# Performance work log

Measured on AMD Instinct MI355X. Metric: run time of the kernel, lower is better.

The kernel has to match this reference:

```python
import jax, jax.numpy as jnp
import numpy as np

EPS = 1e-12  # torch F.normalize eps

def _l2norm(t):
    # normalize over last axis (N), clamp norm like torch.nn.functional.normalize
    n = jnp.linalg.norm(t, axis=-1, keepdims=True)
    return t / jnp.maximum(n, EPS)

def setup_inputs() -> dict:
    key = jax.random.key(0)
    ks = jax.random.split(key, 4)
    B, N, D, H = 8, 4096, 768, 16
    x = jax.random.normal(ks[0], (B, N, D), dtype=jnp.float32)
    w_qkv = jax.random.normal(ks[1], (D, 3 * D), dtype=jnp.float32) * (D ** -0.5)
    temperature = jnp.ones((H, 1, 1), dtype=jnp.float32)
    w_proj = jax.random.normal(ks[2], (D, D), dtype=jnp.float32) * (D ** -0.5)
    b_proj = jnp.zeros((D,), dtype=jnp.float32)
    return {"x": x, "w_qkv": w_qkv, "temperature": temperature,
            "w_proj": w_proj, "b_proj": b_proj}

def reference(x, w_qkv, temperature, w_proj, b_proj):
    B, N, D = x.shape
    H = temperature.shape[0]
    C = D // H
    # qkv linear (no bias), split last dim as (3, H, C), move to (3, B, H, C, N)
    qkv = (x @ w_qkv).reshape(B, N, 3, H, C).transpose(2, 0, 3, 4, 1)
    q, k, v = qkv[0], qkv[1], qkv[2]            # each [B, H, C, N]
    q = _l2norm(q)
    k = _l2norm(k)
    # cross-covariance attention: small CxC matrix per head
    attn = jnp.einsum('bhcn,bhdn->bhcd', q, k) * temperature  # [B,H,C,C]
    attn = jax.nn.softmax(attn, axis=-1)
    out = jnp.einsum('bhcd,bhdn->bhcn', attn, v)  # [B,H,C,N]
    out = out.transpose(0, 3, 1, 2).reshape(B, N, D)  # B N (H C)
    return out @ w_proj + b_proj
```

## Files before the change

### kernel.cpp

```cpp
#include <hip/hip_runtime.h>
#include <stdint.h>

typedef __attribute__((ext_vector_type(4))) float          f32x4;
typedef __attribute__((ext_vector_type(8))) short          bf16x8;
typedef __attribute__((ext_vector_type(8))) unsigned short u16x8;
typedef __attribute__((ext_vector_type(4))) unsigned short u16x4;

static __device__ __forceinline__ unsigned short f2bf(float f){
  uint32_t u = __builtin_bit_cast(uint32_t, f);
  u += 0x7FFFu + ((u >> 16) & 1u);
  return (unsigned short)(u >> 16);
}
static __device__ __forceinline__ float bf2f(unsigned short h){
  uint32_t u = ((uint32_t)h) << 16;
  return __builtin_bit_cast(float, u);
}

#define GLL(SRC, DST) __builtin_amdgcn_global_load_lds(                         \
    (const __attribute__((address_space(1))) unsigned int*)(SRC),               \
    (__attribute__((address_space(3))) unsigned int*)(DST), 16, 0, 0)

__global__ void k_cvt(const float* __restrict__ in, unsigned short* __restrict__ out, long n){
  long i = ((long)blockIdx.x * blockDim.x + threadIdx.x) * 8;
  if (i >= n) return;
  const f32x4* p = (const f32x4*)(in + i);
  f32x4 a = p[0], b = p[1];
  u16x8 o;
  #pragma unroll
  for (int j = 0; j < 4; j++){ o[j] = f2bf(a[j]); o[4+j] = f2bf(b[j]); }
  *(u16x8*)(out + i) = o;
}

__global__ void k_tconv(const float* __restrict__ in, unsigned short* __restrict__ out, int R, int C){
  __shared__ float tl[64][65];
  const int c0 = blockIdx.x * 64, r0 = blockIdx.y * 64;
  const int t = threadIdx.x;
  {
    const int lr = t >> 2, lc = (t & 3) * 16;
    const f32x4* s = (const f32x4*)(in + (long)(r0 + lr) * C + c0 + lc);
    #pragma unroll
    for (int q = 0; q < 4; q++){
      f32x4 v = s[q];
      #pragma unroll
      for (int j = 0; j < 4; j++) tl[lr][lc + q*4 + j] = v[j];
    }
  }
  __syncthreads();
  {
    const int oc = t >> 2, orr = (t & 3) * 16;
    u16x8 o0, o1;
    #pragma unroll
    for (int i = 0; i < 8; i++){ o0[i] = f2bf(tl[orr + i][oc]); o1[i] = f2bf(tl[orr + 8 + i][oc]); }
    u16x8* dst = (u16x8*)(out + (long)(c0 + oc) * R + r0 + orr);
    dst[0] = o0; dst[1] = o1;
  }
}

__global__ void k_cvtwv(const float* __restrict__ w, unsigned short* __restrict__ out){
  const long idx = ((long)blockIdx.x * blockDim.x + threadIdx.x) * 8;
  const int e = (int)(idx / 768), hd = (int)(idx - (long)e * 768);
  const float* s = w + (long)e * 2304 + 1536 + hd;
  f32x4 a = *(const f32x4*)s, b = *(const f32x4*)(s + 4);
  u16x8 o;
  #pragma unroll
  for (int j = 0; j < 4; j++){ o[j] = f2bf(a[j]); o[4+j] = f2bf(b[j]); }
  *(u16x8*)(out + idx) = o;
}

static __device__ __forceinline__ bf16x8 ldfrag(const char* slot, int row, int ko){
  const int k2 = (ko ^ (row >> 1)) & 3;
  return *(const bf16x8*)(slot + row*64 + k2*16);
}

static __device__ __forceinline__ void stg256(const unsigned short* __restrict__ G, int row0, int ke,
                                              char* lds_slot, int t){
  #pragma unroll
  for (int l = 0; l < 2; l++){
    const int r  = l*128 + (t >> 2);
    const int k2 = (t & 3) ^ ((r >> 1) & 3);
    GLL((const char*)(G + (long)(row0 + r) * 768 + ke + k2 * 8),
        lds_slot + l*8192 + (t & 0x1C0) * 16);
  }
}

#define PHASE(BUF, KK, MH, STAGE_STMT, WAIT_STMT) do {                         \
    bf16x8 af[4];                                                              \
    if (MH == 0) {                                                             \
      _Pragma("unroll")                                                        \
      for (int ni = 0; ni < 4; ni++)                                           \
        bq[ni] = ldfrag(sB[BUF][KK], wn*64 + ni*16 + arow, ko);                \
    }                                                                          \
    _Pragma("unroll")                                                          \
    for (int mi = 0; mi < 4; mi++)                                             \
      af[mi] = ldfrag(sA[BUF][KK], wm*128 + MH*64 + mi*16 + arow, ko);         \
    __builtin_amdgcn_s_barrier();                                              \
    __builtin_amdgcn_s_setprio(1);                                             \
    _Pragma("unroll")                                                          \
    for (int mi = 0; mi < 4; mi++)                                             \
      _Pragma("unroll")                                                        \
      for (int ni = 0; ni < 4; ni++)                                           \
        acc[MH*4+mi][ni] = __builtin_amdgcn_mfma_f32_16x16x32_bf16(            \
            af[mi], bq[ni], acc[MH*4+mi][ni], 0, 0, 0);                        \
    __builtin_amdgcn_s_setprio(0);                                             \
    STAGE_STMT;                                                                \
    WAIT_STMT;                                                                 \
    __builtin_amdgcn_s_barrier();                                              \
  } while(0)

__global__ __launch_bounds__(512, 2)
void k_gemm256(const unsigned short* __restrict__ A, const unsigned short* __restrict__ BT,
               unsigned short* __restrict__ QT, unsigned short* __restrict__ KT,
               float* __restrict__ nrmp)
{
  __shared__ __attribute__((aligned(16))) char lds[131072];
  const int o  = blockIdx.x;
  const int wg = (o & 7) * 96 + (o >> 3);
  const int jt = wg % 6, mt = wg / 6;
  const int m0 = mt * 256, j0 = jt * 256;
  const int t = threadIdx.x, lane = t & 63, w = t >> 6;
  const int wm = w >> 2, wn = w & 3;
  const int arow = lane & 15, ko = lane >> 4;

  char* const sA[2][2] = {{lds,           lds + 16384},
                          {lds + 65536,   lds + 65536 + 16384}};
  char* const sB[2][2] = {{lds + 32768,   lds + 49152},
                          {lds + 65536 + 32768, lds + 65536 + 49152}};

  f32x4 acc[8][4] = {};

  stg256(BT, j0, 0,   sB[0][0], t);
  stg256(A,  m0, 0,   sA[0][0], t);
  stg256(BT, j0, 32,  sB[0][1], t);
  stg256(A,  m0, 32,  sA[0][1], t);
  stg256(BT, j0, 64,  sB[1][0], t);
  stg256(A,  m0, 64,  sA[1][0], t);
  stg256(BT, j0, 96,  sB[1][1], t);
  asm volatile("s_waitcnt vmcnt(6)" ::: "memory");
  __builtin_amdgcn_s_barrier();

  #pragma unroll 1
  for (int it = 0; it < 6; ++it){
    const int t1 = 2*it + 1, t2 = 2*it + 2, t3 = 2*it + 3;
    bf16x8 bq[4];
    PHASE(0,0,0, { stg256(A, m0, t1*64+32, sA[1][1], t); }, ;);
    PHASE(0,0,1, { if (t2 < 12) stg256(BT, j0, t2*64,    sB[0][0], t); }, ;);
    PHASE(0,1,0, { if (t2 < 12) stg256(A,  m0, t2*64,    sA[0][0], t); }, ;);
    PHASE(0,1,1, { if (t2 < 12) stg256(BT, j0, t2*64+32, sB[0][1], t); },
                 { if (it == 5) asm volatile("s_waitcnt vmcnt(0)" ::: "memory");
                   else         asm volatile("s_waitcnt vmcnt(6)" ::: "memory"); });
    PHASE(1,0,0, { if (t2 < 12) stg256(A,  m0, t2*64+32, sA[0][1], t); }, ;);
    PHASE(1,0,1, { if (t3 < 12) stg256(BT, j0, t3*64,    sB[1][0], t); }, ;);
    PHASE(1,1,0, { if (t3 < 12) stg256(A,  m0, t3*64,    sA[1][0], t); }, ;);
    PHASE(1,1,1, { if (t3 < 12) stg256(BT, j0, t3*64+32, sB[1][1], t); },
                 { if (it == 5) asm volatile("s_waitcnt vmcnt(0)" ::: "memory");
                   else         asm volatile("s_waitcnt vmcnt(6)" ::: "memory"); });
  }

  const int b = m0 >> 12;
  const int chunk = ((m0 & 4095) >> 7) + wm;
  #pragma unroll
  for (int ni = 0; ni < 4; ni++){
    float ss = 0.f;
    #pragma unroll
    for (int mi = 0; mi < 8; mi++)
      #pragma unroll
      for (int r = 0; r < 4; r++) ss += acc[mi][ni][r] * acc[mi][ni][r];
    ss += __shfl_xor(ss, 16);
    ss += __shfl_xor(ss, 32);
    if (lane < 16){
      const int jc = j0 + wn*64 + ni*16 + lane;
      const int s  = (jc >= 768);
      const int jl = jc - s * 768;
      const int h  = jl / 48;
      const int c  = jl - h * 48;
      nrmp[(long)(s*6144 + (b*16 + h)*48 + c)*32 + chunk] = ss;
    }
  }
  #pragma unroll
  for (int mi = 0; mi < 8; mi++){
    #pragma unroll
    for (int ni = 0; ni < 4; ni++){
      const int j   = wn*64 + ni*16 + (lane & 15);
      const int nb8 = (wm*128 + mi*16 + (lane >> 4)*4) * 2;
      u16x4 pk;
      #pragma unroll
      for (int r = 0; r < 4; r++) pk[r] = f2bf(acc[mi][ni][r]);
      *(u16x4*)(lds + (long)j*512 + (((nb8 >> 3) ^ (j & 7)) << 3)) = pk;
    }
  }
  __syncthreads();
  for (int rr = 0; rr < 32; rr++){
    const int j  = w*32 + rr;
    const int jc = j0 + j;
    const int s  = (jc >= 768);
    const int jl = jc - s * 768;
    const int h  = jl / 48;
    const int c  = jl - h * 48;
    uint2 v = *(const uint2*)(lds + (long)j*512 + ((lane ^ (j & 7)) << 3));
    *(uint2*)((s ? KT : QT) + (((long)(b*16 + h) * 48 + c) << 12) + (m0 & 4095) + lane*4) = v;
  }
}

static __device__ __forceinline__ void stageA512(const unsigned short* __restrict__ G, int row0, int ke,
                                                 char* slot, int t){
  const int r  = t >> 2;
  const int k2 = (t & 3) ^ ((r >> 1) & 3);
  GLL((const char*)(G + (long)(row0 + r) * 768 + ke + k2 * 8), slot + (t & 0x1C0) * 16);
}
static __device__ __forceinline__ void stageB512(const unsigned short* __restrict__ G, int row0, int ke,
                                                 char* slot, int t){
  #pragma unroll
  for (int l = 0; l < 2; l++){
    const int r  = l*128 + (t >> 2);
    const int k2 = (t & 3) ^ ((r >> 1) & 3);
    GLL((const char*)(G + (long)(row0 + r) * 768 + ke + k2 * 8), slot + l*8192 + (t & 0x1C0) * 16);
  }
}

#define VM0 asm volatile("s_waitcnt vmcnt(0)" ::: "memory")
#define VM3 asm volatile("s_waitcnt vmcnt(3)" ::: "memory")

#define PHASE1(CUR, STAGE_STMT, WAIT_STMT) do {                                \
    bf16x8 af[4], bq[4];                                                       \
    _Pragma("unroll")                                                          \
    for (int ni = 0; ni < 4; ni++)                                             \
      bq[ni] = ldfrag(sB[CUR], wn*64 + ni*16 + arow, ko);                      \
    _Pragma("unroll")                                                          \
    for (int mi = 0; mi < 4; mi++)                                             \
      af[mi] = ldfrag(sA[CUR], wm64 + mi*16 + arow, ko);                       \
    __builtin_amdgcn_s_barrier();                                              \
    __builtin_amdgcn_s_setprio(1);                                             \
    _Pragma("unroll")                                                          \
    for (int mi = 0; mi < 4; mi++)                                             \
      _Pragma("unroll")                                                        \
      for (int ni = 0; ni < 4; ni++)                                           \
        acc[mi][ni] = __builtin_amdgcn_mfma_f32_16x16x32_bf16(                 \
            af[mi], bq[ni], acc[mi][ni], 0, 0, 0);                             \
    __builtin_amdgcn_s_setprio(0);                                             \
    STAGE_STMT;                                                                \
    WAIT_STMT;                                                                 \
    __builtin_amdgcn_s_barrier();                                              \
  } while(0)

__global__ __launch_bounds__(512, 4)
void k_gemmP(const unsigned short* __restrict__ A, const unsigned short* __restrict__ BT,
             float* __restrict__ OUTF, const float* __restrict__ bias)
{
  __shared__ __attribute__((aligned(16))) char lds[73728];
  const int o  = blockIdx.x;
  const int wg = (o & 7) * 96 + (o >> 3);
  const int jt = wg % 3, mt = wg / 3;
  const int m0 = mt * 128, j0 = jt * 256;
  const int t = threadIdx.x, lane = t & 63, w = t >> 6;
  const int wm = w >> 2, wn = w & 3;
  const int wm64 = wm * 64;
  const int arow = lane & 15, ko = lane >> 4;
  const unsigned short* BTb = BT + ((long)(m0 >> 12)) * 589824;

  char* const sA[3] = {lds,          lds + 8192,          lds + 16384};
  char* const sB[3] = {lds + 24576,  lds + 24576 + 16384, lds + 24576 + 32768};

  f32x4 acc[4][4] = {};

  stageA512(A, m0, 0,  sA[0], t);  stageB512(BTb, j0, 0,  sB[0], t);
  stageA512(A, m0, 32, sA[1], t);  stageB512(BTb, j0, 32, sB[1], t);
  VM3;
  __builtin_amdgcn_s_barrier();

  #pragma unroll 1
  for (int g = 0; g < 7; ++g){
    const int kb = g * 96;
    PHASE1(0, { stageA512(A, m0, kb+64,  sA[2], t); stageB512(BTb, j0, kb+64,  sB[2], t); }, VM3);
    PHASE1(1, { stageA512(A, m0, kb+96,  sA[0], t); stageB512(BTb, j0, kb+96,  sB[0], t); }, VM3);
    PHASE1(2, { stageA512(A, m0, kb+128, sA[1], t); stageB512(BTb, j0, kb+128, sB[1], t); }, VM3);
  }
  PHASE1(0, { stageA512(A, m0, 736, sA[2], t); stageB512(BTb, j0, 736, sB[2], t); }, VM3);
  PHASE1(1, { ; }, VM0);
  PHASE1(2, { ; }, ;);

  #pragma unroll
  for (int mi = 0; mi < 4; mi++){
    #pragma unroll
    for (int ni = 0; ni < 4; ni++){
      const int jc = j0 + wn*64 + ni*16 + (lane & 15);
      const float bv = bias[jc];
      const long mr = (long)m0 + wm64 + mi*16 + (lane >> 4)*4;
      #pragma unroll
      for (int r = 0; r < 4; r++) OUTF[(mr + r) * 768 + jc] = acc[mi][ni][r] + bv;
    }
  }
}

__global__ __launch_bounds__(256)
void k_attn_part(const unsigned short* __restrict__ QT, const unsigned short* __restrict__ KT,
                 float* __restrict__ Spart)
{
  __shared__ float Sl[4][2304];
  const int bh = blockIdx.x, ksp = blockIdx.y;
  const int t = threadIdx.x, lane = t & 63, w = t >> 6;
  const unsigned short* qb = QT + ((long)bh * 48 << 12);
  const unsigned short* kb = KT + ((long)bh * 48 << 12);
  const int n00 = ksp * 1024 + w * 256;
  f32x4 acc[3][3] = {};
  for (int kt = 0; kt < 256; kt += 32){
    bf16x8 af[3], bfr[3];
    #pragma unroll
    for (int ci = 0; ci < 3; ci++)
      af[ci]  = *(const bf16x8*)(qb + ((long)(ci*16 + (lane & 15)) << 12) + n00 + kt + (lane >> 4) * 8);
    #pragma unroll
    for (int di = 0; di < 3; di++)
      bfr[di] = *(const bf16x8*)(kb + ((long)(di*16 + (lane & 15)) << 12) + n00 + kt + (lane >> 4) * 8);
    #pragma unroll
    for (int ci = 0; ci < 3; ci++)
      #pragma unroll
      for (int di = 0; di < 3; di++)
        acc[ci][di] = __builtin_amdgcn_mfma_f32_16x16x32_bf16(af[ci], bfr[di], acc[ci][di], 0, 0, 0);
  }
  #pragma unroll
  for (int ci = 0; ci < 3; ci++)
    #pragma unroll
    for (int di = 0; di < 3; di++)
      #pragma unroll
      for (int r = 0; r < 4; r++)
        Sl[w][(ci*16 + (lane >> 4)*4 + r) * 48 + di*16 + (lane & 15)] = acc[ci][di][r];
  __syncthreads();
  float* outp = Spart + ((long)ksp * 128 + bh) * 2304;
  for (int idx = t; idx < 2304; idx += 256)
    outp[idx] = Sl[0][idx] + Sl[1][idx] + Sl[2][idx] + Sl[3][idx];
}

__global__ void k_softmax(const float* __restrict__ Spart, const float* __restrict__ nrmp,
                          const float* __restrict__ temp, unsigned short* __restrict__ attnT)
{
  __shared__ float invq[48], invk[48];
  const int bh = blockIdx.x, h = bh & 15;
  const int c = threadIdx.x;
  if (c < 48){
    float sq = 0.f, sk = 0.f;
    const float* pq = nrmp + (long)(bh*48 + c) * 32;
    const float* pk = nrmp + (long)(6144 + bh*48 + c) * 32;
    #pragma unroll
    for (int i = 0; i < 32; i++){ sq += pq[i]; sk += pk[i]; }
    invq[c] = 1.0f / fmaxf(sqrtf(sq), 1e-12f);
    invk[c] = 1.0f / fmaxf(sqrtf(sk), 1e-12f);
  }
  __syncthreads();
  if (c < 48){
    const float scq = invq[c] * temp[h];
    float row[48];
    #pragma unroll
    for (int d = 0; d < 48; d++){
      long base = ((long)bh * 48 + c) * 48 + d;
      float v = Spart[base] + Spart[base + 128L*2304] + Spart[base + 256L*2304] + Spart[base + 384L*2304];
      row[d] = v * scq * invk[d];
    }
    float mx = -1e30f;
    #pragma unroll
    for (int d = 0; d < 48; d++) mx = fmaxf(mx, row[d]);
    float s = 0.f;
    #pragma unroll
    for (int d = 0; d < 48; d++){ row[d] = expf(row[d] - mx); s += row[d]; }
    const float inv = 1.0f / s;
    unsigned short* ob = attnT + (long)bh * 48 * 64;
    #pragma unroll
    for (int d = 0; d < 48; d++) ob[d*64 + c] = f2bf(row[d] * inv);
    u16x8 z = {};
    *(u16x8*)(ob + c*64 + 48) = z;
    *(u16x8*)(ob + c*64 + 56) = z;
  }
}

__global__ __launch_bounds__(256)
void k_wmod2(const unsigned short* __restrict__ WpT, const unsigned short* __restrict__ attnT,
             unsigned short* __restrict__ WmodT)
{
  const int j0 = blockIdx.x * 256, h = blockIdx.y, b = blockIdx.z;
  const int t = threadIdx.x, lane = t & 63, w = t >> 6;
  const unsigned short* wp = WpT + h * 48;
  const unsigned short* ab = attnT + ((long)(b*16 + h)) * 48 * 64;
  f32x4 acc[4][3] = {};
  #pragma unroll
  for (int kt = 0; kt < 64; kt += 32){
    bf16x8 bfr[3];
    #pragma unroll
    for (int ni = 0; ni < 3; ni++)
      bfr[ni] = *(const bf16x8*)(ab + (ni*16 + (lane & 15))*64 + kt + (lane >> 4)*8);
    #pragma unroll
    for (int mi = 0; mi < 4; mi++){
      const int j = j0 + w*64 + mi*16 + (lane & 15);
      bf16x8 a = *(const bf16x8*)(wp + (long)j*768 + kt + (lane >> 4)*8);
      #pragma unroll
      for (int ni = 0; ni < 3; ni++)
        acc[mi][ni] = __builtin_amdgcn_mfma_f32_16x16x32_bf16(a, bfr[ni], acc[mi][ni], 0, 0, 0);
    }
  }
  #pragma unroll
  for (int mi = 0; mi < 4; mi++)
    #pragma unroll
    for (int ni = 0; ni < 3; ni++)
      #pragma unroll
      for (int r = 0; r < 4; r++){
        const int j = j0 + w*64 + mi*16 + (lane >> 4)*4 + r;
        const int d = ni*16 + (lane & 15);
        WmodT[(long)b*589824 + (long)j*768 + h*48 + d] = f2bf(acc[mi][ni][r]);
      }
}

__global__ __launch_bounds__(256)
void k_comb(const unsigned short* __restrict__ A, const unsigned short* __restrict__ BT,
            unsigned short* __restrict__ OUT)
{
  __shared__ unsigned short As[128 * 32];
  __shared__ unsigned short Bs[128 * 32];
  const int m0 = blockIdx.y * 128;
  const int j0 = blockIdx.x * 128;
  const int t = threadIdx.x;
  const int lane = t & 63;
  const int w = t >> 6, wm = w >> 1, wn = w & 1;

  f32x4 acc[4][4] = {};

  for (int kt = 0; kt < 768; kt += 32){
    if (kt) __syncthreads();
    #pragma unroll
    for (int i = 0; i < 2; i++){
      const char* ga = (const char*)A  + (long)(m0 + i*64 + (t >> 2)) * 1536 + kt*2 + (t & 3) * 16;
      const char* gb = (const char*)BT + (long)(j0 + i*64 + (t >> 2)) * 1536 + kt*2 + (t & 3) * 16;
      char* la = (char*)As + i*4096 + (t & 0xC0) * 16;
      char* lb = (char*)Bs + i*4096 + (t & 0xC0) * 16;
      GLL(ga, la);
      GLL(gb, lb);
    }
    __syncthreads();
    bf16x8 af[4], bfr[4];
    #pragma unroll
    for (int mi = 0; mi < 4; mi++)
      af[mi]  = *(const bf16x8*)&As[(wm*64 + mi*16 + (lane & 15)) * 32 + (lane >> 4) * 8];
    #pragma unroll
    for (int ni = 0; ni < 4; ni++)
      bfr[ni] = *(const bf16x8*)&Bs[(wn*64 + ni*16 + (lane & 15)) * 32 + (lane >> 4) * 8];
    #pragma unroll
    for (int mi = 0; mi < 4; mi++)
      #pragma unroll
      for (int ni = 0; ni < 4; ni++)
        acc[mi][ni] = __builtin_amdgcn_mfma_f32_16x16x32_bf16(af[mi], bfr[ni], acc[mi][ni], 0, 0, 0);
  }

  #pragma unroll
  for (int mi = 0; mi < 4; mi++)
    #pragma unroll
    for (int ni = 0; ni < 4; ni++){
      const int jc = j0 + wn*64 + ni*16 + (lane & 15);
      const long mr = (long)m0 + wm*64 + mi*16 + (lane >> 4) * 4;
      #pragma unroll
      for (int r = 0; r < 4; r++) OUT[(mr + r) * 768 + jc] = f2bf(acc[mi][ni][r]);
    }
}

extern "C" void kernel_launch(void* const* d_in, const int* in_sizes, int n_in,
                              void* d_out, int out_size, void* d_ws, size_t ws_size,
                              hipStream_t stream)
{
  (void)in_sizes; (void)n_in; (void)out_size; (void)ws_size;
  const float* x      = (const float*)d_in[0];
  const float* w_qkv  = (const float*)d_in[1];
  const float* temp   = (const float*)d_in[2];
  const float* w_proj = (const float*)d_in[3];
  const float* b_proj = (const float*)d_in[4];
  float* outF = (float*)d_out;

  char* ws = (char*)d_ws;
  size_t off = 0;
  auto alloc = [&](size_t bytes)->char*{ char* p = ws + off; off += (bytes + 255) & ~(size_t)255; return p; };

  unsigned short* x_bf  = (unsigned short*)alloc(50331648);
  unsigned short* WT    = (unsigned short*)alloc(2359296);
  unsigned short* WpT   = (unsigned short*)alloc(1179648);
  unsigned short* WvB   = (unsigned short*)alloc(1179648);
  unsigned short* QT    = (unsigned short*)alloc(100663296);
  unsigned short* KT    = QT + (long)6144 * 4096;
  float* nrmp           = (float*)alloc(12288L * 32 * 4);
  float* Spart          = (float*)alloc(4L * 128 * 2304 * 4);
  unsigned short* attnT = (unsigned short*)alloc(786432);
  unsigned short* WmodT = (unsigned short*)alloc(9437184);
  unsigned short* WcombT= (unsigned short*)alloc(9437184);

  k_cvt<<<12288, 256, 0, stream>>>(x, x_bf, 25165824L);
  k_tconv<<<dim3(24, 12), 256, 0, stream>>>(w_qkv, WT, 768, 2304);
  k_tconv<<<dim3(12, 12), 256, 0, stream>>>(w_proj, WpT, 768, 768);
  k_cvtwv<<<288, 256, 0, stream>>>(w_qkv, WvB);
  k_gemm256<<<768, 512, 0, stream>>>(x_bf, WT, QT, KT, nrmp);
  k_attn_part<<<dim3(128, 4), 256, 0, stream>>>(QT, KT, Spart);
  k_softmax<<<128, 64, 0, stream>>>(Spart, nrmp, temp, attnT);
  k_wmod2<<<dim3(3, 16, 8), 256, 0, stream>>>(WpT, attnT, WmodT);
  k_comb<<<dim3(6, 48), 256, 0, stream>>>(WmodT, WvB, WcombT);
  k_gemmP<<<768, 512, 0, stream>>>(x_bf, WcombT, outF, b_proj);
}
```

Measured before the change: 238.9 us.

## Store Q/K intermediates as FP8 e4m3 and use FP8 MFMA for QK^T

The QKV GEMM epilogue now packs the Q and K outputs into FP8 e4m3 using a software round-to-nearest-even conversion, and the attention partial kernel reads them with the fp8 MFMA. This halves the write and read traffic of the large Q/K intermediate. The two weight transpose-convert launches are also merged into one kernel. The cost is lower precision in the Q·K reduction, since norms are computed separately in fp32, and extra ALU work in the epilogue for the manual conversion.

```diff
diff --git a/kernel.cpp b/kernel.cpp
--- a/kernel.cpp
+++ b/kernel.cpp
@@ -14,6 +14,31 @@
 static __device__ __forceinline__ float bf2f(unsigned short h){
   uint32_t u = ((uint32_t)h) << 16;
   return __builtin_bit_cast(float, u);
+}
+
+static __device__ __forceinline__ uint32_t f2e4m3(float x){
+  uint32_t u = __builtin_bit_cast(uint32_t, x);
+  uint32_t s = (u >> 24) & 0x80u;
+  uint32_t a = u & 0x7FFFFFFFu;
+  if (a >= 0x43E00000u) return s | 0x7Eu;
+  int ebits = (int)(a >> 23);
+  uint32_t mfull = (a & 0x7FFFFFu) | 0x800000u;
+  int shift = (ebits >= 121) ? 20 : 20 + (121 - ebits);
+  if (shift > 31) return s;
+  uint32_t q = mfull >> shift;
+  uint32_t rem = mfull & ((1u << shift) - 1u);
+  uint32_t half = 1u << (shift - 1);
+  q += (rem > half || (rem == half && (q & 1u)));
+  if (ebits >= 121){
+    uint32_t E = (uint32_t)(ebits - 121 + 1);
+    if (q == 16u){ E += 1u; q = 8u; }
+    uint32_t man = q - 8u;
+    if (E > 15u || (E == 15u && man == 7u)) return s | 0x7Eu;
+    return s | (E << 3) | man;
+  } else {
+    if (q >= 8u) return s | (1u << 3) | (q - 8u);
+    return s | q;
+  }
 }
 
 #define GLL(SRC, DST) __builtin_amdgcn_global_load_lds(                         \
@@ -31,9 +56,14 @@
   *(u16x8*)(out + i) = o;
 }
 
-__global__ void k_tconv(const float* __restrict__ in, unsigned short* __restrict__ out, int R, int C){
+__global__ void k_tconv2(const float* __restrict__ wqkv, const float* __restrict__ wproj,
+                         unsigned short* __restrict__ WT, unsigned short* __restrict__ WpT){
   __shared__ float tl[64][65];
-  const int c0 = blockIdx.x * 64, r0 = blockIdx.y * 64;
+  const int bx = blockIdx.x;
+  const float* in = (bx < 24) ? wqkv : wproj;
+  unsigned short* out = (bx < 24) ? WT : WpT;
+  const int C = (bx < 24) ? 2304 : 768;
+  const int c0 = ((bx < 24) ? bx : bx - 24) * 64, r0 = blockIdx.y * 64;
   const int t = threadIdx.x;
   {
     const int lr = t >> 2, lc = (t & 3) * 16;
@@ -51,7 +81,7 @@
     u16x8 o0, o1;
     #pragma unroll
     for (int i = 0; i < 8; i++){ o0[i] = f2bf(tl[orr + i][oc]); o1[i] = f2bf(tl[orr + 8 + i][oc]); }
-    u16x8* dst = (u16x8*)(out + (long)(c0 + oc) * R + r0 + orr);
+    u16x8* dst = (u16x8*)(out + (long)(c0 + oc) * 768 + r0 + orr);
     dst[0] = o0; dst[1] = o1;
   }
 }
@@ -109,7 +139,7 @@
 
 __global__ __launch_bounds__(512, 2)
 void k_gemm256(const unsigned short* __restrict__ A, const unsigned short* __restrict__ BT,
-               unsigned short* __restrict__ QT, unsigned short* __restrict__ KT,
+               unsigned char* __restrict__ QT8, unsigned char* __restrict__ KT8,
                float* __restrict__ nrmp)
 {
   __shared__ __attribute__((aligned(16))) char lds[131072];
@@ -180,12 +210,14 @@
   for (int mi = 0; mi < 8; mi++){
     #pragma unroll
     for (int ni = 0; ni < 4; ni++){
-      const int j   = wn*64 + ni*16 + (lane & 15);
-      const int nb8 = (wm*128 + mi*16 + (lane >> 4)*4) * 2;
-      u16x4 pk;
-      #pragma unroll
-      for (int r = 0; r < 4; r++) pk[r] = f2bf(acc[mi][ni][r]);
-      *(u16x4*)(lds + (long)j*512 + (((nb8 >> 3) ^ (j & 7)) << 3)) = pk;
+      const int j  = wn*64 + ni*16 + (lane & 15);
+      const int nl = wm*128 + mi*16 + (lane >> 4)*4;
+      uint32_t pk =  f2e4m3(acc[mi][ni][0])
+                  | (f2e4m3(acc[mi][ni][1]) << 8)
+                  | (f2e4m3(acc[mi][ni][2]) << 16)
+                  | (f2e4m3(acc[mi][ni][3]) << 24);
+      const int d = (nl >> 2) ^ ((j & 15) << 2);
+      *(uint32_t*)(lds + (long)j*256 + (d << 2)) = pk;
     }
   }
   __syncthreads();
@@ -196,8 +228,9 @@
     const int jl = jc - s * 768;
     const int h  = jl / 48;
     const int c  = jl - h * 48;
-    uint2 v = *(const uint2*)(lds + (long)j*512 + ((lane ^ (j & 7)) << 3));
-    *(uint2*)((s ? KT : QT) + (((long)(b*16 + h) * 48 + c) << 12) + (m0 & 4095) + lane*4) = v;
+    const int dp = lane ^ ((j & 15) << 2);
+    uint32_t v = *(const uint32_t*)(lds + (long)j*256 + (dp << 2));
+    *(uint32_t*)((s ? KT8 : QT8) + ((long)((b*16 + h)*48 + c) << 12) + (m0 & 4095) + lane*4) = v;
   }
 }
 
@@ -292,29 +325,29 @@
 }
 
 __global__ __launch_bounds__(256)
-void k_attn_part(const unsigned short* __restrict__ QT, const unsigned short* __restrict__ KT,
+void k_attn_part(const unsigned char* __restrict__ QT8, const unsigned char* __restrict__ KT8,
                  float* __restrict__ Spart)
 {
   __shared__ float Sl[4][2304];
   const int bh = blockIdx.x, ksp = blockIdx.y;
   const int t = threadIdx.x, lane = t & 63, w = t >> 6;
-  const unsigned short* qb = QT + ((long)bh * 48 << 12);
-  const unsigned short* kb = KT + ((long)bh * 48 << 12);
+  const unsigned char* qb = QT8 + ((long)bh * 48 << 12);
+  const unsigned char* kb = KT8 + ((long)bh * 48 << 12);
   const int n00 = ksp * 1024 + w * 256;
   f32x4 acc[3][3] = {};
   for (int kt = 0; kt < 256; kt += 32){
-    bf16x8 af[3], bfr[3];
+    long af[3], bfr[3];
     #pragma unroll
     for (int ci = 0; ci < 3; ci++)
-      af[ci]  = *(const bf16x8*)(qb + ((long)(ci*16 + (lane & 15)) << 12) + n00 + kt + (lane >> 4) * 8);
+      af[ci]  = *(const long*)(qb + ((long)(ci*16 + (lane & 15)) << 12) + n00 + kt + (lane >> 4) * 8);
     #pragma unroll
     for (int di = 0; di < 3; di++)
-      bfr[di] = *(const bf16x8*)(kb + ((long)(di*16 + (lane & 15)) << 12) + n00 + kt + (lane >> 4) * 8);
+      bfr[di] = *(const long*)(kb + ((long)(di*16 + (lane & 15)) << 12) + n00 + kt + (lane >> 4) * 8);
     #pragma unroll
     for (int ci = 0; ci < 3; ci++)
       #pragma unroll
       for (int di = 0; di < 3; di++)
-        acc[ci][di] = __builtin_amdgcn_mfma_f32_16x16x32_bf16(af[ci], bfr[di], acc[ci][di], 0, 0, 0);
+        acc[ci][di] = __builtin_amdgcn_mfma_f32_16x16x32_fp8_fp8(af[ci], bfr[di], acc[ci][di], 0, 0, 0);
   }
   #pragma unroll
   for (int ci = 0; ci < 3; ci++)
@@ -477,8 +510,8 @@
   unsigned short* WT    = (unsigned short*)alloc(2359296);
   unsigned short* WpT   = (unsigned short*)alloc(1179648);
   unsigned short* WvB   = (unsigned short*)alloc(1179648);
-  unsigned short* QT    = (unsigned short*)alloc(100663296);
-  unsigned short* KT    = QT + (long)6144 * 4096;
+  unsigned char*  QT8   = (unsigned char*)alloc(50331648);
+  unsigned char*  KT8   = QT8 + (long)6144 * 4096;
   float* nrmp           = (float*)alloc(12288L * 32 * 4);
   float* Spart          = (float*)alloc(4L * 128 * 2304 * 4);
   unsigned short* attnT = (unsigned short*)alloc(786432);
@@ -486,11 +519,10 @@
   unsigned short* WcombT= (unsigned short*)alloc(9437184);
 
   k_cvt<<<12288, 256, 0, stream>>>(x, x_bf, 25165824L);
-  k_tconv<<<dim3(24, 12), 256, 0, stream>>>(w_qkv, WT, 768, 2304);
-  k_tconv<<<dim3(12, 12), 256, 0, stream>>>(w_proj, WpT, 768, 768);
+  k_tconv2<<<dim3(36, 12), 256, 0, stream>>>(w_qkv, w_proj, WT, WpT);
   k_cvtwv<<<288, 256, 0, stream>>>(w_qkv, WvB);
-  k_gemm256<<<768, 512, 0, stream>>>(x_bf, WT, QT, KT, nrmp);
-  k_attn_part<<<dim3(128, 4), 256, 0, stream>>>(QT, KT, Spart);
+  k_gemm256<<<768, 512, 0, stream>>>(x_bf, WT, QT8, KT8, nrmp);
+  k_attn_part<<<dim3(128, 4), 256, 0, stream>>>(QT8, KT8, Spart);
   k_softmax<<<128, 64, 0, stream>>>(Spart, nrmp, temp, attnT);
   k_wmod2<<<dim3(3, 16, 8), 256, 0, stream>>>(WpT, attnT, WmodT);
   k_comb<<<dim3(6, 48), 256, 0, stream>>>(WmodT, WvB, WcombT);
```

Result: slower. 307.4 us (+28.7%).
